# Optimization experiments

Hardware: AMD Instinct MI355X
Metric: run time of the kernel (lower is better)

Reference implementation:

```python
import jax, jax.numpy as jnp
import numpy as np

LN_EPS = 1e-5


def _ln(h, g, b):
    mu = h.mean(-1, keepdims=True)
    var = ((h - mu) ** 2).mean(-1, keepdims=True)
    return (h - mu) / jnp.sqrt(var + LN_EPS) * g + b


def setup_inputs() -> dict:
    key = jax.random.key(0)
    ks = jax.random.split(key, 12)
    B, T, Cin, C, D, M = 16, 1024, 512, 1024, 256, 1024
    s = 0.02
    inp = {
        "x": jax.random.normal(ks[0], (B, T, Cin), jnp.float32),
        "masks": jnp.ones((B, T), jnp.float32),
        "W1": jax.random.normal(ks[1], (Cin, C), jnp.float32) * s,
        "g1": jnp.ones((C,), jnp.float32), "b1": jnp.zeros((C,), jnp.float32),
        "W2": jax.random.normal(ks[2], (C, C), jnp.float32) * s,
        "g2": jnp.ones((C,), jnp.float32), "b2": jnp.zeros((C,), jnp.float32),
        "W3": jax.random.normal(ks[3], (C, C), jnp.float32) * s,
        "g3": jnp.ones((C,), jnp.float32), "b3": jnp.zeros((C,), jnp.float32),
        "W4": jax.random.normal(ks[4], (C, C), jnp.float32) * s,
        "g4": jnp.ones((C,), jnp.float32), "b4": jnp.zeros((C,), jnp.float32),
        "W5": jax.random.normal(ks[5], (C, D), jnp.float32) * s,
        "b5": jnp.zeros((D,), jnp.float32),
        # Dirichlet(alpha=100) rows, as in the torch init: rows live on the simplex
        "embedding": jax.random.dirichlet(ks[6], jnp.full((D,), 100.0, jnp.float32), (M,)).astype(jnp.float32),
    }
    return inp


def reference(x, masks, W1, g1, b1, W2, g2, b2, W3, g3, b3, W4, g4, b4, W5, b5, embedding):
    h = jax.nn.relu(_ln(x @ W1, g1, b1))
    h = jax.nn.relu(_ln(h @ W2, g2, b2))
    h = jax.nn.relu(_ln(h @ W3, g3, b3))
    h = jax.nn.relu(_ln(h @ W4, g4, b4))
    z = h @ W5 + b5                              # [B, T, D]
    p = jax.nn.log_softmax(z, axis=-1)           # log-prob features

    B, T, D = p.shape
    p_flat = jax.lax.stop_gradient(p.reshape(-1, D))   # x.detach() in torch
    ep = jnp.exp(p_flat)                               # [N, D]
    # KL(exp(p) || e_m) summed over D, for all codes m:
    #   sum_d exp(p)*(p - log(e_m)) = rowsum(exp(p)*p) - exp(p) @ log(E)^T
    div = (ep * p_flat).sum(-1, keepdims=True) - ep @ jnp.log(embedding).T  # [N, M]
    idx = jnp.argmin(div, axis=-1)                     # [N]
    quant = jax.lax.stop_gradient(embedding[idx].reshape(B, T, D))

    # commitment loss: masked KL(exp(p) || quant.detach())
    kl = (jnp.exp(p) * (p - jnp.log(quant))).sum(-1)   # [B, T]
    loss = 0.25 * (kl * masks).mean(0).sum()

    # straight-through estimator
    q = p + jax.lax.stop_gradient(quant - p)
    return z, q, loss
```

## Files before the change

### kernel.cpp

```cpp
#include <hip/hip_runtime.h>
#include <hip/hip_fp16.h>
#include <stdint.h>

typedef __attribute__((ext_vector_type(4))) float f32x4;
typedef __attribute__((ext_vector_type(2))) float f32x2;
typedef _Float16 f16;
typedef __attribute__((ext_vector_type(8))) _Float16 f16x8;
typedef __attribute__((ext_vector_type(4))) _Float16 f16x4;

#define LN_EPS 1e-5f

__device__ __forceinline__ void gload_lds16(const void* g, void* l) {
  __builtin_amdgcn_global_load_lds(
      (__attribute__((address_space(1))) void*)(uintptr_t)g,
      (__attribute__((address_space(3))) void*)(uint32_t)(uintptr_t)l,
      16, 0, 0);
}

__device__ __forceinline__ f32x4 mfma16(f16x8 a, f16x8 b, f32x4 c) {
  return __builtin_amdgcn_mfma_f32_16x16x32_f16(a, b, c, 0, 0, 0);
}

__device__ __forceinline__ void transpose256(const float* __restrict__ W,
                                             f16* __restrict__ Wt, int K, int N,
                                             int nt, int kt, float (*t)[33]) {
  int tx = threadIdx.x & 31;
  int ty0 = (threadIdx.x >> 5) * 4;
#pragma unroll
  for (int j = 0; j < 4; ++j)
    t[ty0 + j][tx] = W[(size_t)(kt + ty0 + j) * N + nt + tx];
  __syncthreads();
#pragma unroll
  for (int j = 0; j < 4; ++j)
    Wt[(size_t)(nt + ty0 + j) * K + kt + tx] = (f16)t[tx][ty0 + j];
}

__global__ __launch_bounds__(256) void k_prep(
    const float* __restrict__ W1, f16* __restrict__ W1t,
    const float* __restrict__ W2, f16* __restrict__ W2t,
    const float* __restrict__ W3, f16* __restrict__ W3t,
    const float* __restrict__ W4, f16* __restrict__ W4t,
    const float* __restrict__ W5, f16* __restrict__ W5t,
    const float* __restrict__ emb, f16* __restrict__ logE) {
  __shared__ float t[32][33];
  const int b = blockIdx.x;
  if (b < 512) {
    transpose256(W1, W1t, 512, 1024, (b & 31) * 32, (b >> 5) * 32, t);
  } else if (b < 3584) {
    int b3 = b - 512;
    int z = b3 >> 10;
    int b4 = b3 & 1023;
    const float* W = z == 0 ? W2 : (z == 1 ? W3 : W4);
    f16* T = z == 0 ? W2t : (z == 1 ? W3t : W4t);
    transpose256(W, T, 1024, 1024, (b4 & 31) * 32, (b4 >> 5) * 32, t);
  } else if (b < 3840) {
    int b5 = b - 3584;
    transpose256(W5, W5t, 1024, 256, (b5 & 7) * 32, (b5 >> 3) * 32, t);
  } else {
    int i = (b - 3840) * 256 + threadIdx.x;
    logE[i] = (f16)logf(emb[i] * 256.0f);
  }
}

__device__ __forceinline__ void stats_epilogue(char* lds, f32x4 (&acc)[8][4],
                                               f32x2* __restrict__ outPart,
                                               int bm0) {
  const int tid = threadIdx.x;
  const int lane = tid & 63;
  const int wid = tid >> 6;
  const int wm = wid >> 2, wn = wid & 3;
  const int r0 = (lane >> 4) * 4;
  const int cc = lane & 15;
  __builtin_amdgcn_s_barrier();
  float* stp = (float*)lds;
  float* stq = (float*)(lds + 4096);
#pragma unroll
  for (int mi = 0; mi < 8; ++mi) {
#pragma unroll
    for (int j = 0; j < 4; ++j) {
      float s = 0.f, q = 0.f;
#pragma unroll
      for (int ni = 0; ni < 4; ++ni) {
        float v = acc[mi][ni][j];
        s += v; q += v * v;
      }
#pragma unroll
      for (int d = 1; d < 16; d <<= 1) { s += __shfl_xor(s, d); q += __shfl_xor(q, d); }
      if (cc == 0) {
        int rl = wm * 128 + mi * 16 + r0 + j;
        stp[rl * 4 + wn] = s;
        stq[rl * 4 + wn] = q;
      }
    }
  }
  __syncthreads();
  if (tid < 256) {
    float s = stp[tid * 4] + stp[tid * 4 + 1] + stp[tid * 4 + 2] + stp[tid * 4 + 3];
    float q = stq[tid * 4] + stq[tid * 4 + 1] + stq[tid * 4 + 2] + stq[tid * 4 + 3];
    f32x2 pr; pr[0] = s; pr[1] = q;
    outPart[(size_t)(bm0 + tid) * 4 + blockIdx.y] = pr;
  }
}

__device__ __forceinline__ void gemm256_core(
    const f16* __restrict__ A, const f16* __restrict__ Bt,
    char* lds, int bm0, int bn0, int K, f32x4 (&acc)[8][4]) {
  const int tid = threadIdx.x;
  const int lane = tid & 63;
  const int wid = tid >> 6;
  const int wm = wid >> 2;
  const int wn = wid & 3;
  const int NT = K >> 6;

  const int slin = tid * 16;
  const int lrow = slin >> 7;
  const int scol = (slin & 127) ^ ((lrow & 7) << 4);
  const char* Ab = (const char*)A;
  const char* Bb = (const char*)Bt;
  const uint32_t rs = (uint32_t)K * 2;

  const int klo = (lane >> 4) * 16;
  const int sw = (lane & 7) << 4;
  const uint32_t kx0 = (uint32_t)(klo ^ sw);
  const uint32_t kx1 = (uint32_t)((64 + klo) ^ sw);
  const uint32_t abase = (uint32_t)(wm * 128 + (lane & 15)) * 128;
  const uint32_t bbase = (uint32_t)(wn * 64 + (lane & 15)) * 128;

#pragma unroll
  for (int i = 0; i < 8; ++i)
#pragma unroll
    for (int j = 0; j < 4; ++j) acc[i][j] = 0.0f;

#define LDSA(buf) (lds + (buf)*32768)
#define LDSB(buf) (lds + 65536 + (buf)*32768)
#define STAGE_A(t, h)                                                              \
  {                                                                                \
    const char* src = Ab + (size_t)(bm0 + (h)*128 + lrow) * rs + ((t) << 7) + scol;\
    char* dst = LDSA((t)&1) + (h)*16384 + slin;                                    \
    gload_lds16(src, dst);                                                         \
    gload_lds16(src + (size_t)64 * rs, dst + 8192);                                \
  }
#define STAGE_B(t, h)                                                              \
  {                                                                                \
    const char* src = Bb + (size_t)(bn0 + (h)*128 + lrow) * rs + ((t) << 7) + scol;\
    char* dst = LDSB((t)&1) + (h)*16384 + slin;                                    \
    gload_lds16(src, dst);                                                         \
    gload_lds16(src + (size_t)64 * rs, dst + 8192);                                \
  }
#define HALF1(Acur, Bcur)                                                          \
  _Pragma("unroll") for (int ni = 0; ni < 4; ++ni) {                               \
    bF[ni][0] = *(const f16x8*)((Bcur) + bbase + ni * 2048 + kx0);                 \
    bF[ni][1] = *(const f16x8*)((Bcur) + bbase + ni * 2048 + kx1);                 \
  }                                                                                \
  {                                                                                \
    f16x8 aF[4][2];                                                                \
    _Pragma("unroll") for (int mi = 0; mi < 4; ++mi) {                             \
      aF[mi][0] = *(const f16x8*)((Acur) + abase + mi * 2048 + kx0);               \
      aF[mi][1] = *(const f16x8*)((Acur) + abase + mi * 2048 + kx1);               \
    }                                                                              \
    __builtin_amdgcn_s_setprio(1);                                                 \
    _Pragma("unroll") for (int mi = 0; mi < 4; ++mi)                               \
        _Pragma("unroll") for (int ni = 0; ni < 4; ++ni) {                         \
          acc[mi][ni] = mfma16(aF[mi][0], bF[ni][0], acc[mi][ni]);                 \
          acc[mi][ni] = mfma16(aF[mi][1], bF[ni][1], acc[mi][ni]);                 \
        }                                                                          \
    __builtin_amdgcn_s_setprio(0);                                                 \
  }
#define HALF2(Acur)                                                                \
  {                                                                                \
    f16x8 aF[4][2];                                                                \
    _Pragma("unroll") for (int mi = 0; mi < 4; ++mi) {                             \
      aF[mi][0] = *(const f16x8*)((Acur) + abase + (mi + 4) * 2048 + kx0);         \
      aF[mi][1] = *(const f16x8*)((Acur) + abase + (mi + 4) * 2048 + kx1);         \
    }                                                                              \
    __builtin_amdgcn_s_setprio(1);                                                 \
    _Pragma("unroll") for (int mi = 0; mi < 4; ++mi)                               \
        _Pragma("unroll") for (int ni = 0; ni < 4; ++ni) {                         \
          acc[mi + 4][ni] = mfma16(aF[mi][0], bF[ni][0], acc[mi + 4][ni]);         \
          acc[mi + 4][ni] = mfma16(aF[mi][1], bF[ni][1], acc[mi + 4][ni]);         \
        }                                                                          \
    __builtin_amdgcn_s_setprio(0);                                                 \
  }

  STAGE_A(0, 0); STAGE_A(0, 1); STAGE_B(0, 0); STAGE_B(0, 1);
  STAGE_B(1, 0); STAGE_B(1, 1);
  asm volatile("s_waitcnt vmcnt(4)");
  __builtin_amdgcn_s_barrier();
  __builtin_amdgcn_sched_barrier(0);

  f16x8 bF[4][2];
  for (int t = 0; t < NT - 2; ++t) {
    const char* Acur = LDSA(t & 1);
    const char* Bcur = LDSB(t & 1);
    STAGE_A(t + 1, 0); STAGE_A(t + 1, 1);
    HALF1(Acur, Bcur)
    __builtin_amdgcn_s_barrier();
    __builtin_amdgcn_sched_barrier(0);
    STAGE_B(t + 2, 0); STAGE_B(t + 2, 1);
    HALF2(Acur)
    asm volatile("s_waitcnt vmcnt(4)");
    __builtin_amdgcn_s_barrier();
    __builtin_amdgcn_sched_barrier(0);
  }
  {
    const char* Acur = LDSA((NT - 2) & 1);
    const char* Bcur = LDSB((NT - 2) & 1);
    STAGE_A(NT - 1, 0); STAGE_A(NT - 1, 1);
    HALF1(Acur, Bcur)
    __builtin_amdgcn_s_barrier();
    __builtin_amdgcn_sched_barrier(0);
    HALF2(Acur)
    asm volatile("s_waitcnt vmcnt(0)");
    __builtin_amdgcn_s_barrier();
    __builtin_amdgcn_sched_barrier(0);
  }
  {
    const char* Acur = LDSA((NT - 1) & 1);
    const char* Bcur = LDSB((NT - 1) & 1);
    HALF1(Acur, Bcur)
    HALF2(Acur)
  }
#undef STAGE_A
#undef HALF1
#undef HALF2
#undef LDSA
#undef LDSB
#undef STAGE_B
}

__global__ __launch_bounds__(512, 2) void k_gemm256_div(
    const f16* __restrict__ A, const f16* __restrict__ Bt,
    float* __restrict__ part_val, int* __restrict__ part_idx, int N, int K) {
  __shared__ char lds[131072];
  const int bm0 = blockIdx.x * 256;
  const int bn0 = blockIdx.y * 256;
  f32x4 acc[8][4];
  gemm256_core(A, Bt, lds, bm0, bn0, K, acc);

  const int lane = threadIdx.x & 63;
  const int wid = threadIdx.x >> 6;
  const int wm = wid >> 2, wn = wid & 3;
  const int r0 = (lane >> 4) * 4;
  const int cc = lane & 15;
  const int nch = N >> 6;
  const int chunk = (bn0 >> 6) + wn;
#pragma unroll
  for (int mi = 0; mi < 8; ++mi) {
#pragma unroll
    for (int j = 0; j < 4; ++j) {
      float v = acc[mi][0][j];
      int c = cc;
#pragma unroll
      for (int ni = 1; ni < 4; ++ni) {
        float v2 = acc[mi][ni][j];
        int c2 = ni * 16 + cc;
        if (v2 > v) { v = v2; c = c2; }
      }
#pragma unroll
      for (int d = 1; d < 16; d <<= 1) {
        float ov = __shfl_xor(v, d);
        int oc = __shfl_xor(c, d);
        if (ov > v || (ov == v && oc < c)) { v = ov; c = oc; }
      }
      if (cc == 0) {
        int r = bm0 + wm * 128 + mi * 16 + r0 + j;
        part_val[r * nch + chunk] = v;
        part_idx[r * nch + chunk] = bn0 + wn * 64 + c;
      }
    }
  }
}

__global__ __launch_bounds__(512, 2) void k_gemm256_cvt(
    const float* __restrict__ A, const f16* __restrict__ Bt,
    f16* __restrict__ O, f32x2* __restrict__ outPart, int N, int K) {
  __shared__ char lds[131072];
  const int tid = threadIdx.x;
  const int lane = tid & 63;
  const int wid = tid >> 6;
  const int wm = wid >> 2;
  const int wn = wid & 3;
  const int bm0 = blockIdx.x * 256;
  const int bn0 = blockIdx.y * 256;
  const int NT = K >> 6;

  const int slin = tid * 16;
  const int lrow = slin >> 7;
  const int scol = (slin & 127) ^ ((lrow & 7) << 4);
  const char* Ab = (const char*)A;
  const char* Bb = (const char*)Bt;
  const uint32_t rsA = (uint32_t)K * 4;
  const uint32_t rs = (uint32_t)K * 2;

  const int klo = (lane >> 4) * 16;
  const int sw = (lane & 7) << 4;
  const uint32_t kx0 = (uint32_t)(klo ^ sw);
  const uint32_t kx1 = (uint32_t)((64 + klo) ^ sw);
  const uint32_t abase = (uint32_t)(wm * 128 + (lane & 15)) * 128;
  const uint32_t bbase = (uint32_t)(wn * 64 + (lane & 15)) * 128;

  const int alrow = tid >> 3;
  const uint32_t acolbF = (uint32_t)(tid & 7) * 32;
  const uint32_t awcol = ((uint32_t)(tid & 7) * 16) ^ (uint32_t)((alrow & 7) << 4);
  f32x4 arf[4][2];

  f32x4 acc[8][4];
#pragma unroll
  for (int i = 0; i < 8; ++i)
#pragma unroll
    for (int j = 0; j < 4; ++j) acc[i][j] = 0.0f;

#define LDSA(buf) (lds + (buf)*32768)
#define LDSB(buf) (lds + 65536 + (buf)*32768)
#define STAGE_B(t, h)                                                              \
  {                                                                                \
    const char* src = Bb + (size_t)(bn0 + (h)*128 + lrow) * rs + ((t) << 7) + scol;\
    char* dst = LDSB((t)&1) + (h)*16384 + slin;                                    \
    gload_lds16(src, dst);                                                         \
    gload_lds16(src + (size_t)64 * rs, dst + 8192);                                \
  }
#define A_ISSUE(t1)                                                               \
  {                                                                               \
    const char* base_ = Ab + (size_t)(bm0 + alrow) * rsA + ((size_t)(t1) << 8) + acolbF; \
    _Pragma("unroll") for (int i = 0; i < 4; ++i) {                               \
      arf[i][0] = *(const f32x4*)(base_ + (size_t)(i * 64) * rsA);                \
      arf[i][1] = *(const f32x4*)(base_ + (size_t)(i * 64) * rsA + 16);           \
    }                                                                             \
  }
#define A_WRITE(t1)                                                               \
  {                                                                               \
    char* wb_ = LDSA((t1)&1);                                                     \
    _Pragma("unroll") for (int i = 0; i < 4; ++i) {                               \
      f16x8 o;                                                                    \
      _Pragma("unroll") for (int e = 0; e < 4; ++e) {                             \
        o[e] = (f16)arf[i][0][e];                                                 \
        o[e + 4] = (f16)arf[i][1][e];                                             \
      }                                                                           \
      *(f16x8*)(wb_ + (i >> 1) * 16384 + (alrow + (i & 1) * 64) * 128 + awcol) = o; \
    }                                                                             \
  }
#define HALF1(Acur, Bcur)                                                          \
  _Pragma("unroll") for (int ni = 0; ni < 4; ++ni) {                               \
    bF[ni][0] = *(const f16x8*)((Bcur) + bbase + ni * 2048 + kx0);                 \
    bF[ni][1] = *(const f16x8*)((Bcur) + bbase + ni * 2048 + kx1);                 \
  }                                                                                \
  {                                                                                \
    f16x8 aF[4][2];                                                                \
    _Pragma("unroll") for (int mi = 0; mi < 4; ++mi) {                             \
      aF[mi][0] = *(const f16x8*)((Acur) + abase + mi * 2048 + kx0);               \
      aF[mi][1] = *(const f16x8*)((Acur) + abase + mi * 2048 + kx1);               \
    }                                                                              \
    __builtin_amdgcn_s_setprio(1);                                                 \
    _Pragma("unroll") for (int mi = 0; mi < 4; ++mi)                               \
        _Pragma("unroll") for (int ni = 0; ni < 4; ++ni) {                         \
          acc[mi][ni] = mfma16(aF[mi][0], bF[ni][0], acc[mi][ni]);                 \
          acc[mi][ni] = mfma16(aF[mi][1], bF[ni][1], acc[mi][ni]);                 \
        }                                                                          \
    __builtin_amdgcn_s_setprio(0);                                                 \
  }
#define HALF2(Acur)                                                                \
  {                                                                                \
    f16x8 aF[4][2];                                                                \
    _Pragma("unroll") for (int mi = 0; mi < 4; ++mi) {                             \
      aF[mi][0] = *(const f16x8*)((Acur) + abase + (mi + 4) * 2048 + kx0);         \
      aF[mi][1] = *(const f16x8*)((Acur) + abase + (mi + 4) * 2048 + kx1);         \
    }                                                                              \
    __builtin_amdgcn_s_setprio(1);                                                 \
    _Pragma("unroll") for (int mi = 0; mi < 4; ++mi)                               \
        _Pragma("unroll") for (int ni = 0; ni < 4; ++ni) {                         \
          acc[mi + 4][ni] = mfma16(aF[mi][0], bF[ni][0], acc[mi + 4][ni]);         \
          acc[mi + 4][ni] = mfma16(aF[mi][1], bF[ni][1], acc[mi + 4][ni]);         \
        }                                                                          \
    __builtin_amdgcn_s_setprio(0);                                                 \
  }

  A_ISSUE(0)
  STAGE_B(0, 0); STAGE_B(0, 1); STAGE_B(1, 0); STAGE_B(1, 1);
  asm volatile("s_waitcnt vmcnt(8)");
  A_WRITE(0)
  asm volatile("s_waitcnt vmcnt(4) lgkmcnt(0)");
  __builtin_amdgcn_s_barrier();
  __builtin_amdgcn_sched_barrier(0);

  f16x8 bF[4][2];
  for (int t = 0; t < NT - 2; ++t) {
    const char* Acur = LDSA(t & 1);
    const char* Bcur = LDSB(t & 1);
    A_ISSUE(t + 1)
    HALF1(Acur, Bcur)
    __builtin_amdgcn_s_barrier();
    __builtin_amdgcn_sched_barrier(0);
    STAGE_B(t + 2, 0); STAGE_B(t + 2, 1);
    HALF2(Acur)
    asm volatile("s_waitcnt vmcnt(4)");
    A_WRITE(t + 1)
    asm volatile("s_waitcnt lgkmcnt(0)");
    __builtin_amdgcn_s_barrier();
    __builtin_amdgcn_sched_barrier(0);
  }
  {
    const char* Acur = LDSA((NT - 2) & 1);
    const char* Bcur = LDSB((NT - 2) & 1);
    A_ISSUE(NT - 1)
    HALF1(Acur, Bcur)
    __builtin_amdgcn_s_barrier();
    __builtin_amdgcn_sched_barrier(0);
    HALF2(Acur)
    asm volatile("s_waitcnt vmcnt(0)");
    A_WRITE(NT - 1)
    asm volatile("s_waitcnt lgkmcnt(0)");
    __builtin_amdgcn_s_barrier();
    __builtin_amdgcn_sched_barrier(0);
  }
  {
    const char* Acur = LDSA((NT - 1) & 1);
    const char* Bcur = LDSB((NT - 1) & 1);
    HALF1(Acur, Bcur)
    HALF2(Acur)
  }
#undef STAGE_B
#undef A_ISSUE
#undef A_WRITE
#undef HALF1
#undef HALF2
#undef LDSA
#undef LDSB

  stats_epilogue(lds, acc, outPart, bm0);

  const int r0 = (lane >> 4) * 4;
  const int cc = lane & 15;
#pragma unroll
  for (int mi = 0; mi < 8; ++mi) {
#pragma unroll
    for (int ni = 0; ni < 4; ++ni) {
      int r = bm0 + wm * 128 + mi * 16 + r0;
      int c = bn0 + wn * 64 + ni * 16 + cc;
#pragma unroll
      for (int j = 0; j < 4; ++j)
        O[(size_t)(r + j) * N + c] = (f16)acc[mi][ni][j];
    }
  }
}

__global__ __launch_bounds__(512, 2) void k_gemm256_ln(
    const f16* __restrict__ A, const f16* __restrict__ Bt,
    f16* __restrict__ O, const float* __restrict__ gw,
    const float* __restrict__ bw, const f32x2* __restrict__ inPart,
    f32x2* __restrict__ outPart, int N, int K) {
  __shared__ char lds[135168];
  const int GB = 131072;
  const int tid = threadIdx.x;
  const int lane = tid & 63;
  const int wid = tid >> 6;
  const int wm = wid >> 2;
  const int wn = wid & 3;
  const int bm0 = blockIdx.x * 256;
  const int bn0 = blockIdx.y * 256;
  const int NT = K >> 6;

  const int slin = tid * 16;
  const int lrow = slin >> 7;
  const int scol = (slin & 127) ^ ((lrow & 7) << 4);
  const char* Ab = (const char*)A;
  const char* Bb = (const char*)Bt;
  const uint32_t rs = (uint32_t)K * 2;

  const int klo = (lane >> 4) * 16;
  const int sw = (lane & 7) << 4;
  const uint32_t kx0 = (uint32_t)(klo ^ sw);
  const uint32_t kx1 = (uint32_t)((64 + klo) ^ sw);
  const uint32_t abase = (uint32_t)(wm * 128 + (lane & 15)) * 128;
  const uint32_t bbase = (uint32_t)(wn * 64 + (lane & 15)) * 128;

  const int alrow = tid >> 3;
  const uint32_t acolb = (uint32_t)(tid & 7) * 16;
  const uint32_t awcol = acolb ^ (uint32_t)((alrow & 7) << 4);
  f16 aSh[4], cSh[4];
  f16x8 ar[4];

  f32x4 acc[8][4];
#pragma unroll
  for (int i = 0; i < 8; ++i)
#pragma unroll
    for (int j = 0; j < 4; ++j) acc[i][j] = 0.0f;

#define LDSA(buf) (lds + (buf)*32768)
#define LDSB(buf) (lds + 65536 + (buf)*32768)
#define STAGE_B(t, h)                                                              \
  {                                                                                \
    const char* src = Bb + (size_t)(bn0 + (h)*128 + lrow) * rs + ((t) << 7) + scol;\
    char* dst = LDSB((t)&1) + (h)*16384 + slin;                                    \
    gload_lds16(src, dst);                                                         \
    gload_lds16(src + (size_t)64 * rs, dst + 8192);                                \
  }
#define A_ISSUE(t1)                                                               \
  {                                                                               \
    const char* base_ = Ab + (size_t)(bm0 + alrow) * rs + ((size_t)(t1) << 7) + acolb; \
    ar[0] = *(const f16x8*)(base_);                                               \
    ar[1] = *(const f16x8*)(base_ + (size_t)64 * rs);                             \
    ar[2] = *(const f16x8*)(base_ + (size_t)128 * rs);                            \
    ar[3] = *(const f16x8*)(base_ + (size_t)192 * rs);                            \
  }
#define A_WRITE(t1)                                                               \
  {                                                                               \
    uint32_t off_ = GB + (uint32_t)(t1)*128 + (uint32_t)(tid & 7) * 16;           \
    f16x8 gr = *(const f16x8*)(lds + off_);                                       \
    f16x8 br = *(const f16x8*)(lds + off_ + 2048);                                \
    char* wb_ = LDSA((t1)&1);                                                     \
    _Pragma("unroll") for (int i = 0; i < 4; ++i) {                               \
      f16x8 aS8, cS8, zz;                                                         \
      _Pragma("unroll") for (int p = 0; p < 8; ++p) {                             \
        aS8[p] = aSh[i]; cS8[p] = cSh[i]; zz[p] = (f16)0.f;                       \
      }                                                                           \
      f16x8 tt = ar[i] * aS8 + cS8;                                               \
      tt = tt * gr + br;                                                          \
      tt = __builtin_elementwise_max(tt, zz);                                     \
      *(f16x8*)(wb_ + (i >> 1) * 16384 + (alrow + (i & 1) * 64) * 128 + awcol) = tt; \
    }                                                                             \
  }

  if (tid < 256) {
    f32x4 g4 = ((const f32x4*)gw)[tid];
    f32x4 b4 = ((const f32x4*)bw)[tid];
    f16x4 gh, bh;
#pragma unroll
    for (int e = 0; e < 4; ++e) { gh[e] = (f16)g4[e]; bh[e] = (f16)b4[e]; }
    ((f16x4*)(lds + GB))[tid] = gh;
    ((f16x4*)(lds + GB + 2048))[tid] = bh;
  }
#pragma unroll
  for (int i = 0; i < 4; ++i) {
    int r = bm0 + (i >> 1) * 128 + (i & 1) * 64 + alrow;
    const f32x4* pp = (const f32x4*)(inPart + (size_t)r * 4);
    f32x4 p0 = pp[0], p1 = pp[1];
    float s = p0[0] + p0[2] + p1[0] + p1[2];
    float q = p0[1] + p0[3] + p1[1] + p1[3];
    float mu = s * (1.0f / 1024.0f);
    float var = q * (1.0f / 1024.0f) - mu * mu;
    float rstd = rsqrtf(var + LN_EPS);
    aSh[i] = (f16)rstd;
    cSh[i] = (f16)(-mu * rstd);
  }
  __builtin_amdgcn_sched_barrier(0);
  A_ISSUE(0)
  STAGE_B(0, 0); STAGE_B(0, 1); STAGE_B(1, 0); STAGE_B(1, 1);
  __builtin_amdgcn_sched_barrier(0);
  asm volatile("s_waitcnt lgkmcnt(0)");
  __builtin_amdgcn_s_barrier();
  asm volatile("s_waitcnt vmcnt(8)");
  A_WRITE(0)
  asm volatile("s_waitcnt vmcnt(4) lgkmcnt(0)");
  __builtin_amdgcn_s_barrier();
  __builtin_amdgcn_sched_barrier(0);

  for (int t = 0; t < NT; ++t) {
    const char* Acur = LDSA(t & 1);
    const char* Bcur = LDSB(t & 1);

    if (t + 1 < NT) { A_ISSUE(t + 1) }
    f16x8 bF[4][2];
#pragma unroll
    for (int ni = 0; ni < 4; ++ni) {
      bF[ni][0] = *(const f16x8*)(Bcur + bbase + ni * 2048 + kx0);
      bF[ni][1] = *(const f16x8*)(Bcur + bbase + ni * 2048 + kx1);
    }
    {
      f16x8 aF[4][2];
#pragma unroll
      for (int mi = 0; mi < 4; ++mi) {
        aF[mi][0] = *(const f16x8*)(Acur + abase + mi * 2048 + kx0);
        aF[mi][1] = *(const f16x8*)(Acur + abase + mi * 2048 + kx1);
      }
      __builtin_amdgcn_s_setprio(1);
#pragma unroll
      for (int mi = 0; mi < 4; ++mi)
#pragma unroll
        for (int ni = 0; ni < 4; ++ni) {
          acc[mi][ni] = mfma16(aF[mi][0], bF[ni][0], acc[mi][ni]);
          acc[mi][ni] = mfma16(aF[mi][1], bF[ni][1], acc[mi][ni]);
        }
      __builtin_amdgcn_s_setprio(0);
    }
    __builtin_amdgcn_s_barrier();
    __builtin_amdgcn_sched_barrier(0);

    if (t + 2 < NT) { STAGE_B(t + 2, 0); STAGE_B(t + 2, 1); }
    {
      f16x8 aF[4][2];
#pragma unroll
      for (int mi = 0; mi < 4; ++mi) {
        aF[mi][0] = *(const f16x8*)(Acur + abase + (mi + 4) * 2048 + kx0);
        aF[mi][1] = *(const f16x8*)(Acur + abase + (mi + 4) * 2048 + kx1);
      }
      __builtin_amdgcn_s_setprio(1);
#pragma unroll
      for (int mi = 0; mi < 4; ++mi)
#pragma unroll
        for (int ni = 0; ni < 4; ++ni) {
          acc[mi + 4][ni] = mfma16(aF[mi][0], bF[ni][0], acc[mi + 4][ni]);
          acc[mi + 4][ni] = mfma16(aF[mi][1], bF[ni][1], acc[mi + 4][ni]);
        }
      __builtin_amdgcn_s_setprio(0);
    }
    if (t + 1 < NT) {
      if (t + 2 < NT) { asm volatile("s_waitcnt vmcnt(4)"); }
      else            { asm volatile("s_waitcnt vmcnt(0)"); }
      A_WRITE(t + 1)
      asm volatile("s_waitcnt lgkmcnt(0)");
      __builtin_amdgcn_s_barrier();
      __builtin_amdgcn_sched_barrier(0);
    }
  }
#undef STAGE_B
#undef A_ISSUE
#undef A_WRITE
#undef LDSA
#undef LDSB

  stats_epilogue(lds, acc, outPart, bm0);

  const int r0 = (lane >> 4) * 4;
  const int cc = lane & 15;
#pragma unroll
  for (int mi = 0; mi < 8; ++mi) {
#pragma unroll
    for (int ni = 0; ni < 4; ++ni) {
      int r = bm0 + wm * 128 + mi * 16 + r0;
      int c = bn0 + wn * 64 + ni * 16 + cc;
#pragma unroll
      for (int j = 0; j < 4; ++j)
        O[(size_t)(r + j) * N + c] = (f16)acc[mi][ni][j];
    }
  }
}

__global__ __launch_bounds__(256) void k_gemm_sm(
    const f16* __restrict__ A, const f16* __restrict__ Bt,
    const float* __restrict__ gw, const float* __restrict__ bw,
    const f32x2* __restrict__ inPart, const float* __restrict__ bias,
    float* __restrict__ z, f16* __restrict__ ep, float* __restrict__ sm) {
  const int K = 1024;
  __shared__ char lds[77824];
  const int GBS = 73728;
  char* ldsA = lds;
  const int tid = threadIdx.x;
  const int lane = tid & 63;
  const int wn = tid >> 6;
  const int bm0 = blockIdx.x * 64;
  const char* Ab = (const char*)A;
  const char* Bb = (const char*)Bt;
  const uint32_t rs = (uint32_t)K * 2;
  const int cc = lane & 15;

  {
    f32x4 g4 = ((const f32x4*)gw)[tid];
    f32x4 b4 = ((const f32x4*)bw)[tid];
    f16x4 gh, bh;
#pragma unroll
    for (int e = 0; e < 4; ++e) { gh[e] = (f16)g4[e]; bh[e] = (f16)b4[e]; }
    ((f16x4*)(lds + GBS))[tid] = gh;
    ((f16x4*)(lds + GBS + 2048))[tid] = bh;
  }

  const int ar0 = tid >> 3;
  f16 aSh[2], cSh[2];
#pragma unroll
  for (int i = 0; i < 2; ++i) {
    int r = bm0 + ar0 + i * 32;
    const f32x4* pp = (const f32x4*)(inPart + (size_t)r * 4);
    f32x4 p0 = pp[0], p1 = pp[1];
    float s = p0[0] + p0[2] + p1[0] + p1[2];
    float q = p0[1] + p0[3] + p1[1] + p1[3];
    float mu = s * (1.0f / 1024.0f);
    float var = q * (1.0f / 1024.0f) - mu * mu;
    float rstd = rsqrtf(var + LN_EPS);
    aSh[i] = (f16)rstd;
    cSh[i] = (f16)(-mu * rstd);
  }
  const uint32_t acolb = (uint32_t)(tid & 7) * 16;
  const uint32_t awcol = acolb ^ (uint32_t)((ar0 & 7) << 4);

  uint32_t ra[2][4], rb[2][4];
  {
    const int sww = (lane & 7) << 4;
    const int gk = lane & 48;
#pragma unroll
    for (int kk = 0; kk < 2; ++kk) {
#pragma unroll
      for (int i = 0; i < 4; ++i) {
        uint32_t kb = (uint32_t)((kk * 64 + gk) ^ sww);
        ra[kk][i] = (uint32_t)(i * 16 + cc) * 128 + kb;
        rb[kk][i] = (uint32_t)(wn * 64 + i * 16 + cc) * 128 + kb;
      }
    }
  }

  f32x4 acc[4][4];
#pragma unroll
  for (int i = 0; i < 4; ++i)
#pragma unroll
    for (int j = 0; j < 4; ++j) acc[i][j] = 0.0f;

#define STAGE_BS(t)                                                               \
  {                                                                               \
    char* bdst = lds + 8192 + ((t)&1) * 32768;                                    \
    _Pragma("unroll") for (int i = 0; i < 8; ++i) {                               \
      int lin = i * 4096 + tid * 16;                                              \
      int row = lin >> 7;                                                         \
      int col = (lin & 127) ^ ((row & 7) << 4);                                   \
      gload_lds16(Bb + (size_t)row * rs + ((size_t)(t) << 7) + col, bdst + lin);  \
    }                                                                             \
  }

  STAGE_BS(0)
  asm volatile("s_waitcnt lgkmcnt(0)");
  __builtin_amdgcn_s_barrier();
  __builtin_amdgcn_sched_barrier(0);

  for (int t = 0; t < 16; ++t) {
    const char* abase_ = Ab + (size_t)(bm0 + ar0) * rs + ((size_t)t << 7) + acolb;
    f16x8 a0 = *(const f16x8*)abase_;
    f16x8 a1 = *(const f16x8*)(abase_ + (size_t)32 * rs);
    if (t + 1 < 16) { STAGE_BS(t + 1) }
    if (t + 1 < 16) { asm volatile("s_waitcnt vmcnt(8)"); }
    else            { asm volatile("s_waitcnt vmcnt(0)"); }
    {
      uint32_t off_ = GBS + (uint32_t)t * 128 + (uint32_t)(tid & 7) * 16;
      f16x8 gr = *(const f16x8*)(lds + off_);
      f16x8 br = *(const f16x8*)(lds + off_ + 2048);
      f16x8 aS0, cS0, aS1, cS1, zz;
#pragma unroll
      for (int p = 0; p < 8; ++p) {
        aS0[p] = aSh[0]; cS0[p] = cSh[0];
        aS1[p] = aSh[1]; cS1[p] = cSh[1];
        zz[p] = (f16)0.f;
      }
      f16x8 t0 = a0 * aS0 + cS0;
      f16x8 t1 = a1 * aS1 + cS1;
      t0 = t0 * gr + br;
      t1 = t1 * gr + br;
      t0 = __builtin_elementwise_max(t0, zz);
      t1 = __builtin_elementwise_max(t1, zz);
      *(f16x8*)(ldsA + ar0 * 128 + awcol) = t0;
      *(f16x8*)(ldsA + (ar0 + 32) * 128 + awcol) = t1;
    }
    asm volatile("s_waitcnt lgkmcnt(0)");
    __builtin_amdgcn_s_barrier();
    __builtin_amdgcn_sched_barrier(0);
    {
      const char* Bcur = lds + 8192 + (t & 1) * 32768;
#pragma unroll
      for (int kk = 0; kk < 2; ++kk) {
        f16x8 af[4], bfv[4];
#pragma unroll
        for (int i = 0; i < 4; ++i) af[i] = *(const f16x8*)(ldsA + ra[kk][i]);
#pragma unroll
        for (int i = 0; i < 4; ++i) bfv[i] = *(const f16x8*)(Bcur + rb[kk][i]);
#pragma unroll
        for (int mi = 0; mi < 4; ++mi)
#pragma unroll
          for (int ni = 0; ni < 4; ++ni)
            acc[mi][ni] = mfma16(af[mi], bfv[ni], acc[mi][ni]);
      }
    }
    __builtin_amdgcn_s_barrier();
    __builtin_amdgcn_sched_barrier(0);
  }
#undef STAGE_BS

  __syncthreads();
  float* stm = (float*)lds;
  float* sts = (float*)(lds + 1024);
  float* rowm = (float*)(lds + 2048);
  float* rows_ = (float*)(lds + 2304);

  const int r0 = (lane >> 4) * 4;
  float bvv[4];
#pragma unroll
  for (int ni = 0; ni < 4; ++ni) bvv[ni] = bias[wn * 64 + ni * 16 + cc];

#pragma unroll
  for (int mi = 0; mi < 4; ++mi) {
#pragma unroll
    for (int j = 0; j < 4; ++j) {
      float m = -3.4e38f;
#pragma unroll
      for (int ni = 0; ni < 4; ++ni) m = fmaxf(m, acc[mi][ni][j] + bvv[ni]);
#pragma unroll
      for (int d = 1; d < 16; d <<= 1) m = fmaxf(m, __shfl_xor(m, d));
      if (cc == 0) stm[wn * 64 + mi * 16 + r0 + j] = m;
    }
  }
  __syncthreads();
  if (tid < 64) {
    float m = fmaxf(fmaxf(stm[tid], stm[64 + tid]), fmaxf(stm[128 + tid], stm[192 + tid]));
    rowm[tid] = m;
  }
  __syncthreads();
#pragma unroll
  for (int mi = 0; mi < 4; ++mi) {
#pragma unroll
    for (int j = 0; j < 4; ++j) {
      int r = mi * 16 + r0 + j;
      float m = rowm[r];
      float s = 0.f;
#pragma unroll
      for (int ni = 0; ni < 4; ++ni) s += expf(acc[mi][ni][j] + bvv[ni] - m);
#pragma unroll
      for (int d = 1; d < 16; d <<= 1) s += __shfl_xor(s, d);
      if (cc == 0) sts[wn * 64 + r] = s;
    }
  }
  __syncthreads();
  if (tid < 64) {
    float s = sts[tid] + sts[64 + tid] + sts[128 + tid] + sts[192 + tid];
    rows_[tid] = s;
    sm[bm0 + tid] = rowm[tid] + logf(s);
  }
  __syncthreads();
#pragma unroll
  for (int mi = 0; mi < 4; ++mi) {
#pragma unroll
    for (int j = 0; j < 4; ++j) {
      int r = mi * 16 + r0 + j;
      float m = rowm[r];
      float inv = 1.0f / rows_[r];
      float* zp = z + (size_t)(bm0 + r) * 256;
      f16* epp = ep + (size_t)(bm0 + r) * 256;
#pragma unroll
      for (int ni = 0; ni < 4; ++ni) {
        int c = wn * 64 + ni * 16 + cc;
        float zz = acc[mi][ni][j] + bvv[ni];
        zp[c] = zz;
        epp[c] = (f16)(expf(zz - m) * inv);
      }
    }
  }
}

__global__ __launch_bounds__(256) void k_final(
    const float* __restrict__ part_val, const int* __restrict__ part_idx,
    const float* __restrict__ z, const float* __restrict__ sm,
    const float* __restrict__ emb, const float* __restrict__ masks,
    float* __restrict__ q, float* __restrict__ blockloss) {
  __shared__ float ls[4];
  int lane = threadIdx.x & 63;
  int w = threadIdx.x >> 6;
  int row = blockIdx.x * 4 + w;
  float v = -3.4e38f;
  int c = 0x7fffffff;
  if (lane < 16) { v = part_val[row * 16 + lane]; c = part_idx[row * 16 + lane]; }
#pragma unroll
  for (int d = 1; d < 16; d <<= 1) {
    float ov = __shfl_xor(v, d);
    int oc = __shfl_xor(c, d);
    if (ov > v || (ov == v && oc < c)) { v = ov; c = oc; }
  }
  int code = __shfl(c, 0);
  f32x4 ev = ((const f32x4*)(emb + (size_t)code * 256))[lane];
  ((f32x4*)(q + (size_t)row * 256))[lane] = ev;
  f32x4 zv = ((const f32x4*)(z + (size_t)row * 256))[lane];
  float smr = sm[row];
  float kl = 0.f;
#pragma unroll
  for (int j = 0; j < 4; ++j) {
    float pj = zv[j] - smr;
    kl += expf(pj) * (pj - logf(ev[j]));
  }
#pragma unroll
  for (int d = 1; d < 64; d <<= 1) kl += __shfl_xor(kl, d);
  if (lane == 0) ls[w] = kl * masks[row];
  __syncthreads();
  if (threadIdx.x == 0) blockloss[blockIdx.x] = ls[0] + ls[1] + ls[2] + ls[3];
}

__global__ __launch_bounds__(256) void k_loss_reduce(const float* __restrict__ bl,
                                                     float* __restrict__ out) {
  __shared__ float s[256];
  float a = 0.f;
#pragma unroll
  for (int i = 0; i < 16; ++i) a += bl[threadIdx.x + i * 256];
  s[threadIdx.x] = a;
  __syncthreads();
  for (int st = 128; st > 0; st >>= 1) {
    if (threadIdx.x < st) s[threadIdx.x] += s[threadIdx.x + st];
    __syncthreads();
  }
  if (threadIdx.x == 0) out[0] = s[0] * (0.25f / 16.0f);
}

extern "C" void kernel_launch(void* const* d_in, const int* in_sizes, int n_in,
                              void* d_out, int out_size, void* d_ws, size_t ws_size,
                              hipStream_t stream) {
  const float* x = (const float*)d_in[0];
  const float* masks = (const float*)d_in[1];
  const float* W1 = (const float*)d_in[2];
  const float* g1 = (const float*)d_in[3];
  const float* b1 = (const float*)d_in[4];
  const float* W2 = (const float*)d_in[5];
  const float* g2 = (const float*)d_in[6];
  const float* b2 = (const float*)d_in[7];
  const float* W3 = (const float*)d_in[8];
  const float* g3 = (const float*)d_in[9];
  const float* b3 = (const float*)d_in[10];
  const float* W4 = (const float*)d_in[11];
  const float* g4 = (const float*)d_in[12];
  const float* b4 = (const float*)d_in[13];
  const float* W5 = (const float*)d_in[14];
  const float* b5 = (const float*)d_in[15];
  const float* emb = (const float*)d_in[16];

  const int M = 16384;
  char* ws = (char*)d_ws;
  f16* bufA = (f16*)(ws);
  f16* bufB = (f16*)(ws + (32ull << 20));
  f16* W1t = (f16*)(ws + (64ull << 20));
  f16* W2t = (f16*)(ws + (65ull << 20));
  f16* W3t = (f16*)(ws + (67ull << 20));
  f16* W4t = (f16*)(ws + (69ull << 20));
  f16* W5t = (f16*)(ws + (71ull << 20));
  f16* logE = (f16*)(ws + (72ull << 20));
  float* part_val = (float*)(ws + (73ull << 20));
  int* part_idx = (int*)(ws + (74ull << 20));
  float* blockloss = (float*)(ws + (75ull << 20));
  float* sm = (float*)(ws + (76ull << 20));
  f32x2* partA = (f32x2*)(ws + (77ull << 20));
  f32x2* partB = (f32x2*)(ws + (78ull << 20));
  f16* ep = (f16*)(ws + (16ull << 20));

  float* z = (float*)d_out;
  float* q = z + (size_t)M * 256;
  float* lossp = z + 2ull * M * 256;

  k_prep<<<4864, 256, 0, stream>>>(W1, W1t, W2, W2t, W3, W3t, W4, W4t,
                                   W5, W5t, emb, logE);
  k_gemm256_cvt<<<dim3(64, 4), 512, 0, stream>>>(x, W1t, bufA, partA, 1024, 512);
  k_gemm256_ln<<<dim3(64, 4), 512, 0, stream>>>(bufA, W2t, bufB, g1, b1, partA, partB, 1024, 1024);
  k_gemm256_ln<<<dim3(64, 4), 512, 0, stream>>>(bufB, W3t, bufA, g2, b2, partB, partA, 1024, 1024);
  k_gemm256_ln<<<dim3(64, 4), 512, 0, stream>>>(bufA, W4t, bufB, g3, b3, partA, partB, 1024, 1024);
  k_gemm_sm<<<256, 256, 0, stream>>>(bufB, W5t, g4, b4, partB, b5, z, ep, sm);
  k_gemm256_div<<<dim3(64, 4), 512, 0, stream>>>(ep, logE, part_val, part_idx, 1024, 256);
  k_final<<<4096, 256, 0, stream>>>(part_val, part_idx, z, sm, emb, masks, q, blockloss);
  k_loss_reduce<<<1, 256, 0, stream>>>(blockloss, lossp);
}
```

Before: 241.9 us.

## Shrink LN-fused GEMM tiles to 128x128 with 256 threads for more blocks

Replaces the 256x256 tile, 512-thread LayerNorm-fused GEMM with a 128x128, 256-thread version, raising the grid from 256 to 1024 blocks and halving LDS per block. The per-row statistic partials now have 8 column slots instead of 4, and the first GEMM zero-fills the unused slots so the consumers can always sum 8. The aim is better CU coverage and occupancy on a 16K x 1024 problem where 256 big tiles leave CUs underused, at the cost of lower per-tile data reuse and more global traffic for A and B.

```diff
diff --git a/kernel.cpp b/kernel.cpp
--- a/kernel.cpp
+++ b/kernel.cpp
@@ -19,6 +19,19 @@
 
 __device__ __forceinline__ f32x4 mfma16(f16x8 a, f16x8 b, f32x4 c) {
   return __builtin_amdgcn_mfma_f32_16x16x32_f16(a, b, c, 0, 0, 0);
+}
+
+__device__ __forceinline__ void ln_coeff(const f32x2* __restrict__ inPart, int r,
+                                         float* rstd_o, float* shift_o) {
+  const f32x4* pp = (const f32x4*)(inPart + (size_t)r * 8);
+  f32x4 p0 = pp[0], p1 = pp[1], p2 = pp[2], p3 = pp[3];
+  float s = p0[0] + p0[2] + p1[0] + p1[2] + p2[0] + p2[2] + p3[0] + p3[2];
+  float q = p0[1] + p0[3] + p1[1] + p1[3] + p2[1] + p2[3] + p3[1] + p3[3];
+  float mu = s * (1.0f / 1024.0f);
+  float var = q * (1.0f / 1024.0f) - mu * mu;
+  float rstd = rsqrtf(var + LN_EPS);
+  *rstd_o = rstd;
+  *shift_o = -mu * rstd;
 }
 
 __device__ __forceinline__ void transpose256(const float* __restrict__ W,
@@ -62,9 +75,9 @@
   }
 }
 
-__device__ __forceinline__ void stats_epilogue(char* lds, f32x4 (&acc)[8][4],
-                                               f32x2* __restrict__ outPart,
-                                               int bm0) {
+__device__ __forceinline__ void stats_epilogue8(char* lds, f32x4 (&acc)[8][4],
+                                                f32x2* __restrict__ outPart,
+                                                int bm0, int zfill) {
   const int tid = threadIdx.x;
   const int lane = tid & 63;
   const int wid = tid >> 6;
@@ -98,7 +111,12 @@
     float s = stp[tid * 4] + stp[tid * 4 + 1] + stp[tid * 4 + 2] + stp[tid * 4 + 3];
     float q = stq[tid * 4] + stq[tid * 4 + 1] + stq[tid * 4 + 2] + stq[tid * 4 + 3];
     f32x2 pr; pr[0] = s; pr[1] = q;
-    outPart[(size_t)(bm0 + tid) * 4 + blockIdx.y] = pr;
+    outPart[(size_t)(bm0 + tid) * 8 + blockIdx.y] = pr;
+    if (zfill && blockIdx.y == 0) {
+      f32x2 zz; zz[0] = 0.f; zz[1] = 0.f;
+#pragma unroll
+      for (int k = 4; k < 8; ++k) outPart[(size_t)(bm0 + tid) * 8 + k] = zz;
+    }
   }
 }
 
@@ -426,7 +444,7 @@
 #undef LDSA
 #undef LDSB
 
-  stats_epilogue(lds, acc, outPart, bm0);
+  stats_epilogue8(lds, acc, outPart, bm0, 1);
 
   const int r0 = (lane >> 4) * 4;
   const int cc = lane & 15;
@@ -443,25 +461,22 @@
   }
 }
 
-__global__ __launch_bounds__(512, 2) void k_gemm256_ln(
+__global__ __launch_bounds__(256, 2) void k_gemm128_ln(
     const f16* __restrict__ A, const f16* __restrict__ Bt,
     f16* __restrict__ O, const float* __restrict__ gw,
     const float* __restrict__ bw, const f32x2* __restrict__ inPart,
     f32x2* __restrict__ outPart, int N, int K) {
-  __shared__ char lds[135168];
-  const int GB = 131072;
+  __shared__ char lds[69632];
+  const int GB = 65536;
   const int tid = threadIdx.x;
   const int lane = tid & 63;
   const int wid = tid >> 6;
-  const int wm = wid >> 2;
-  const int wn = wid & 3;
-  const int bm0 = blockIdx.x * 256;
-  const int bn0 = blockIdx.y * 256;
+  const int wm = wid >> 1;
+  const int wn = wid & 1;
+  const int bm0 = blockIdx.x * 128;
+  const int bn0 = blockIdx.y * 128;
   const int NT = K >> 6;
 
-  const int slin = tid * 16;
-  const int lrow = slin >> 7;
-  const int scol = (slin & 127) ^ ((lrow & 7) << 4);
   const char* Ab = (const char*)A;
   const char* Bb = (const char*)Bt;
   const uint32_t rs = (uint32_t)K * 2;
@@ -470,7 +485,7 @@
   const int sw = (lane & 7) << 4;
   const uint32_t kx0 = (uint32_t)(klo ^ sw);
   const uint32_t kx1 = (uint32_t)((64 + klo) ^ sw);
-  const uint32_t abase = (uint32_t)(wm * 128 + (lane & 15)) * 128;
+  const uint32_t abase = (uint32_t)(wm * 64 + (lane & 15)) * 128;
   const uint32_t bbase = (uint32_t)(wn * 64 + (lane & 15)) * 128;
 
   const int alrow = tid >> 3;
@@ -479,28 +494,32 @@
   f16 aSh[4], cSh[4];
   f16x8 ar[4];
 
-  f32x4 acc[8][4];
-#pragma unroll
-  for (int i = 0; i < 8; ++i)
+  f32x4 acc[4][4];
+#pragma unroll
+  for (int i = 0; i < 4; ++i)
 #pragma unroll
     for (int j = 0; j < 4; ++j) acc[i][j] = 0.0f;
 
-#define LDSA(buf) (lds + (buf)*32768)
-#define LDSB(buf) (lds + 65536 + (buf)*32768)
-#define STAGE_B(t, h)                                                              \
-  {                                                                                \
-    const char* src = Bb + (size_t)(bn0 + (h)*128 + lrow) * rs + ((t) << 7) + scol;\
-    char* dst = LDSB((t)&1) + (h)*16384 + slin;                                    \
-    gload_lds16(src, dst);                                                         \
-    gload_lds16(src + (size_t)64 * rs, dst + 8192);                                \
+#define LDSA(buf) (lds + (buf)*16384)
+#define LDSB(buf) (lds + 32768 + (buf)*16384)
+#define STAGE_B(t)                                                                \
+  {                                                                               \
+    char* bdst = LDSB((t)&1);                                                     \
+    _Pragma("unroll") for (int i = 0; i < 4; ++i) {                               \
+      int lin = i * 4096 + tid * 16;                                              \
+      int row = lin >> 7;                                                         \
+      int col = (lin & 127) ^ ((row & 7) << 4);                                   \
+      gload_lds16(Bb + (size_t)(bn0 + row) * rs + ((size_t)(t) << 7) + col,       \
+                  bdst + lin);                                                    \
+    }                                                                             \
   }
 #define A_ISSUE(t1)                                                               \
   {                                                                               \
     const char* base_ = Ab + (size_t)(bm0 + alrow) * rs + ((size_t)(t1) << 7) + acolb; \
     ar[0] = *(const f16x8*)(base_);                                               \
-    ar[1] = *(const f16x8*)(base_ + (size_t)64 * rs);                             \
-    ar[2] = *(const f16x8*)(base_ + (size_t)128 * rs);                            \
-    ar[3] = *(const f16x8*)(base_ + (size_t)192 * rs);                            \
+    ar[1] = *(const f16x8*)(base_ + (size_t)32 * rs);                             \
+    ar[2] = *(const f16x8*)(base_ + (size_t)64 * rs);                             \
+    ar[3] = *(const f16x8*)(base_ + (size_t)96 * rs);                             \
   }
 #define A_WRITE(t1)                                                               \
   {                                                                               \
@@ -516,11 +535,45 @@
       f16x8 tt = ar[i] * aS8 + cS8;                                               \
       tt = tt * gr + br;                                                          \
       tt = __builtin_elementwise_max(tt, zz);                                     \
-      *(f16x8*)(wb_ + (i >> 1) * 16384 + (alrow + (i & 1) * 64) * 128 + awcol) = tt; \
+      *(f16x8*)(wb_ + (alrow + i * 32) * 128 + awcol) = tt;                       \
     }                                                                             \
   }
-
-  if (tid < 256) {
+#define HALF1(Acur, Bcur)                                                          \
+  _Pragma("unroll") for (int ni = 0; ni < 4; ++ni) {                               \
+    bF[ni][0] = *(const f16x8*)((Bcur) + bbase + ni * 2048 + kx0);                 \
+    bF[ni][1] = *(const f16x8*)((Bcur) + bbase + ni * 2048 + kx1);                 \
+  }                                                                                \
+  {                                                                                \
+    f16x8 aF[2][2];                                                                \
+    _Pragma("unroll") for (int mi = 0; mi < 2; ++mi) {                             \
+      aF[mi][0] = *(const f16x8*)((Acur) + abase + mi * 2048 + kx0);               \
+      aF[mi][1] = *(const f16x8*)((Acur) + abase + mi * 2048 + kx1);               \
+    }                                                                              \
+    __builtin_amdgcn_s_setprio(1);                                                 \
+    _Pragma("unroll") for (int mi = 0; mi < 2; ++mi)                               \
+        _Pragma("unroll") for (int ni = 0; ni < 4; ++ni) {                         \
+          acc[mi][ni] = mfma16(aF[mi][0], bF[ni][0], acc[mi][ni]);                 \
+          acc[mi][ni] = mfma16(aF[mi][1], bF[ni][1], acc[mi][ni]);                 \
+        }                                                                          \
+    __builtin_amdgcn_s_setprio(0);                                                 \
+  }
+#define HALF2(Acur)                                                                \
+  {                                                                                \
+    f16x8 aF[2][2];                                                                \
+    _Pragma("unroll") for (int mi = 0; mi < 2; ++mi) {                             \
+      aF[mi][0] = *(const f16x8*)((Acur) + abase + (mi + 2) * 2048 + kx0);         \
+      aF[mi][1] = *(const f16x8*)((Acur) + abase + (mi + 2) * 2048 + kx1);         \
+    }                                                                              \
+    __builtin_amdgcn_s_setprio(1);                                                 \
+    _Pragma("unroll") for (int mi = 0; mi < 2; ++mi)                               \
+        _Pragma("unroll") for (int ni = 0; ni < 4; ++ni) {                         \
+          acc[mi + 2][ni] = mfma16(aF[mi][0], bF[ni][0], acc[mi + 2][ni]);         \
+          acc[mi + 2][ni] = mfma16(aF[mi][1], bF[ni][1], acc[mi + 2][ni]);         \
+        }                                                                          \
+    __builtin_amdgcn_s_setprio(0);                                                 \
+  }
+
+  {
     f32x4 g4 = ((const f32x4*)gw)[tid];
     f32x4 b4 = ((const f32x4*)bw)[tid];
     f16x4 gh, bh;
@@ -531,20 +584,14 @@
   }
 #pragma unroll
   for (int i = 0; i < 4; ++i) {
-    int r = bm0 + (i >> 1) * 128 + (i & 1) * 64 + alrow;
-    const f32x4* pp = (const f32x4*)(inPart + (size_t)r * 4);
-    f32x4 p0 = pp[0], p1 = pp[1];
-    float s = p0[0] + p0[2] + p1[0] + p1[2];
-    float q = p0[1] + p0[3] + p1[1] + p1[3];
-    float mu = s * (1.0f / 1024.0f);
-    float var = q * (1.0f / 1024.0f) - mu * mu;
-    float rstd = rsqrtf(var + LN_EPS);
+    float rstd, shift;
+    ln_coeff(inPart, bm0 + alrow + i * 32, &rstd, &shift);
     aSh[i] = (f16)rstd;
-    cSh[i] = (f16)(-mu * rstd);
+    cSh[i] = (f16)shift;
   }
   __builtin_amdgcn_sched_barrier(0);
   A_ISSUE(0)
-  STAGE_B(0, 0); STAGE_B(0, 1); STAGE_B(1, 0); STAGE_B(1, 1);
+  STAGE_B(0) STAGE_B(1)
   __builtin_amdgcn_sched_barrier(0);
   asm volatile("s_waitcnt lgkmcnt(0)");
   __builtin_amdgcn_s_barrier();
@@ -554,55 +601,18 @@
   __builtin_amdgcn_s_barrier();
   __builtin_amdgcn_sched_barrier(0);
 
+  f16x8 bF[4][2];
   for (int t = 0; t < NT; ++t) {
     const char* Acur = LDSA(t & 1);
     const char* Bcur = LDSB(t & 1);
 
     if (t + 1 < NT) { A_ISSUE(t + 1) }
-    f16x8 bF[4][2];
-#pragma unroll
-    for (int ni = 0; ni < 4; ++ni) {
-      bF[ni][0] = *(const f16x8*)(Bcur + bbase + ni * 2048 + kx0);
-      bF[ni][1] = *(const f16x8*)(Bcur + bbase + ni * 2048 + kx1);
-    }
-    {
-      f16x8 aF[4][2];
-#pragma unroll
-      for (int mi = 0; mi < 4; ++mi) {
-        aF[mi][0] = *(const f16x8*)(Acur + abase + mi * 2048 + kx0);
-        aF[mi][1] = *(const f16x8*)(Acur + abase + mi * 2048 + kx1);
-      }
-      __builtin_amdgcn_s_setprio(1);
-#pragma unroll
-      for (int mi = 0; mi < 4; ++mi)
-#pragma unroll
-        for (int ni = 0; ni < 4; ++ni) {
-          acc[mi][ni] = mfma16(aF[mi][0], bF[ni][0], acc[mi][ni]);
-          acc[mi][ni] = mfma16(aF[mi][1], bF[ni][1], acc[mi][ni]);
-        }
-      __builtin_amdgcn_s_setprio(0);
-    }
-    __builtin_amdgcn_s_barrier();
-    __builtin_amdgcn_sched_barrier(0);
-
-    if (t + 2 < NT) { STAGE_B(t + 2, 0); STAGE_B(t + 2, 1); }
-    {
-      f16x8 aF[4][2];
-#pragma unroll
-      for (int mi = 0; mi < 4; ++mi) {
-        aF[mi][0] = *(const f16x8*)(Acur + abase + (mi + 4) * 2048 + kx0);
-        aF[mi][1] = *(const f16x8*)(Acur + abase + (mi + 4) * 2048 + kx1);
-      }
-      __builtin_amdgcn_s_setprio(1);
-#pragma unroll
-      for (int mi = 0; mi < 4; ++mi)
-#pragma unroll
-        for (int ni = 0; ni < 4; ++ni) {
-          acc[mi + 4][ni] = mfma16(aF[mi][0], bF[ni][0], acc[mi + 4][ni]);
-          acc[mi + 4][ni] = mfma16(aF[mi][1], bF[ni][1], acc[mi + 4][ni]);
-        }
-      __builtin_amdgcn_s_setprio(0);
-    }
+    HALF1(Acur, Bcur)
+    __builtin_amdgcn_s_barrier();
+    __builtin_amdgcn_sched_barrier(0);
+
+    if (t + 2 < NT) { STAGE_B(t + 2) }
+    HALF2(Acur)
     if (t + 1 < NT) {
       if (t + 2 < NT) { asm volatile("s_waitcnt vmcnt(4)"); }
       else            { asm volatile("s_waitcnt vmcnt(0)"); }
@@ -615,18 +625,50 @@
 #undef STAGE_B
 #undef A_ISSUE
 #undef A_WRITE
+#undef HALF1
+#undef HALF2
 #undef LDSA
 #undef LDSB
 
-  stats_epilogue(lds, acc, outPart, bm0);
-
   const int r0 = (lane >> 4) * 4;
   const int cc = lane & 15;
-#pragma unroll
-  for (int mi = 0; mi < 8; ++mi) {
+  __builtin_amdgcn_s_barrier();
+  {
+    float* stp = (float*)lds;
+    float* stq = (float*)(lds + 1024);
+#pragma unroll
+    for (int mi = 0; mi < 4; ++mi) {
+#pragma unroll
+      for (int j = 0; j < 4; ++j) {
+        float s = 0.f, q = 0.f;
+#pragma unroll
+        for (int ni = 0; ni < 4; ++ni) {
+          float v = acc[mi][ni][j];
+          s += v; q += v * v;
+        }
+#pragma unroll
+        for (int d = 1; d < 16; d <<= 1) { s += __shfl_xor(s, d); q += __shfl_xor(q, d); }
+        if (cc == 0) {
+          int rl = wm * 64 + mi * 16 + r0 + j;
+          stp[rl * 2 + wn] = s;
+          stq[rl * 2 + wn] = q;
+        }
+      }
+    }
+    __syncthreads();
+    if (tid < 128) {
+      float s = stp[tid * 2] + stp[tid * 2 + 1];
+      float q = stq[tid * 2] + stq[tid * 2 + 1];
+      f32x2 pr; pr[0] = s; pr[1] = q;
+      outPart[(size_t)(bm0 + tid) * 8 + blockIdx.y] = pr;
+    }
+  }
+
+#pragma unroll
+  for (int mi = 0; mi < 4; ++mi) {
 #pragma unroll
     for (int ni = 0; ni < 4; ++ni) {
-      int r = bm0 + wm * 128 + mi * 16 + r0;
+      int r = bm0 + wm * 64 + mi * 16 + r0;
       int c = bn0 + wn * 64 + ni * 16 + cc;
 #pragma unroll
       for (int j = 0; j < 4; ++j)
@@ -667,16 +709,10 @@
   f16 aSh[2], cSh[2];
 #pragma unroll
   for (int i = 0; i < 2; ++i) {
-    int r = bm0 + ar0 + i * 32;
-    const f32x4* pp = (const f32x4*)(inPart + (size_t)r * 4);
-    f32x4 p0 = pp[0], p1 = pp[1];
-    float s = p0[0] + p0[2] + p1[0] + p1[2];
-    float q = p0[1] + p0[3] + p1[1] + p1[3];
-    float mu = s * (1.0f / 1024.0f);
-    float var = q * (1.0f / 1024.0f) - mu * mu;
-    float rstd = rsqrtf(var + LN_EPS);
+    float rstd, shift;
+    ln_coeff(inPart, bm0 + ar0 + i * 32, &rstd, &shift);
     aSh[i] = (f16)rstd;
-    cSh[i] = (f16)(-mu * rstd);
+    cSh[i] = (f16)shift;
   }
   const uint32_t acolb = (uint32_t)(tid & 7) * 16;
   const uint32_t awcol = acolb ^ (uint32_t)((ar0 & 7) << 4);
@@ -936,9 +972,9 @@
   k_prep<<<4864, 256, 0, stream>>>(W1, W1t, W2, W2t, W3, W3t, W4, W4t,
                                    W5, W5t, emb, logE);
   k_gemm256_cvt<<<dim3(64, 4), 512, 0, stream>>>(x, W1t, bufA, partA, 1024, 512);
-  k_gemm256_ln<<<dim3(64, 4), 512, 0, stream>>>(bufA, W2t, bufB, g1, b1, partA, partB, 1024, 1024);
-  k_gemm256_ln<<<dim3(64, 4), 512, 0, stream>>>(bufB, W3t, bufA, g2, b2, partB, partA, 1024, 1024);
-  k_gemm256_ln<<<dim3(64, 4), 512, 0, stream>>>(bufA, W4t, bufB, g3, b3, partA, partB, 1024, 1024);
+  k_gemm128_ln<<<dim3(128, 8), 256, 0, stream>>>(bufA, W2t, bufB, g1, b1, partA, partB, 1024, 1024);
+  k_gemm128_ln<<<dim3(128, 8), 256, 0, stream>>>(bufB, W3t, bufA, g2, b2, partB, partA, 1024, 1024);
+  k_gemm128_ln<<<dim3(128, 8), 256, 0, stream>>>(bufA, W4t, bufB, g3, b3, partA, partB, 1024, 1024);
   k_gemm_sm<<<256, 256, 0, stream>>>(bufB, W5t, g4, b4, partB, b5, z, ep, sm);
   k_gemm256_div<<<dim3(64, 4), 512, 0, stream>>>(ep, logE, part_val, part_idx, 1024, 256);
   k_final<<<4096, 256, 0, stream>>>(part_val, part_idx, z, sm, emb, masks, q, blockloss);
```

New measurement: 267.2 us. 10.5% more time.
